# Kernel tuning notes

Measured on AMD Instinct MI355X. Metric: run time of the kernel, lower is better.

The kernel has to match this reference:

```python
import jax, jax.numpy as jnp
import numpy as np

N_NODES = 50000
N_EDGES = 800000
ORIG_FEA = 92
NBR_FEA = 41
HID = 64
N_CONV = 3
BN_EPS = 1e-5


def setup_inputs() -> dict:
    key = jax.random.key(0)
    ks = jax.random.split(key, 16)
    s = 0.05
    inp = {
        "x": jax.random.normal(ks[0], (N_NODES, ORIG_FEA), dtype=jnp.float32),
        "edge_attr": jax.random.normal(ks[1], (N_EDGES, NBR_FEA), dtype=jnp.float32),
        "edge_index": jax.random.randint(ks[2], (2, N_EDGES), 0, N_NODES, dtype=jnp.int64),
        # embedding1 / embedding2
        "W1": jax.random.normal(ks[3], (ORIG_FEA, HID), dtype=jnp.float32) * s,
        "b1": jnp.zeros((HID,), dtype=jnp.float32),
        "W2": jax.random.normal(ks[4], (NBR_FEA, HID), dtype=jnp.float32) * s,
        "b2": jnp.zeros((HID,), dtype=jnp.float32),
        # CGConv lin_f / lin_s per layer, stacked [n_conv, 3*HID, HID]
        "Wf": jax.random.normal(ks[5], (N_CONV, 3 * HID, HID), dtype=jnp.float32) * s,
        "bf": jnp.zeros((N_CONV, HID), dtype=jnp.float32),
        "Ws": jax.random.normal(ks[6], (N_CONV, 3 * HID, HID), dtype=jnp.float32) * s,
        "bs": jnp.zeros((N_CONV, HID), dtype=jnp.float32),
        # BatchNorm1d per layer (training mode: batch statistics)
        "gamma": jnp.ones((N_CONV, HID), dtype=jnp.float32),
        "beta": jnp.zeros((N_CONV, HID), dtype=jnp.float32),
    }
    return inp


def _cgconv(x, e, src, tgt, Wf, bf, Ws, bs):
    # z_ij = [x_i (target), x_j (source), e_ij]  -> [E, 3H]
    z = jnp.concatenate([x[tgt], x[src], e], axis=-1)
    gate = jax.nn.sigmoid(z @ Wf + bf)
    core = jax.nn.softplus(z @ Ws + bs)
    msg = gate * core  # [E, H]
    agg = jax.ops.segment_sum(msg, tgt, num_segments=x.shape[0])
    return x + agg  # residual


def _batchnorm(x, gamma, beta):
    mean = jnp.mean(x, axis=0)
    var = jnp.mean(jnp.square(x - mean), axis=0)  # biased var (torch BN training)
    return (x - mean) * jax.lax.rsqrt(var + BN_EPS) * gamma + beta


def reference(x, edge_attr, edge_index, W1, b1, W2, b2, Wf, bf, Ws, bs, gamma, beta):
    src, tgt = edge_index[0], edge_index[1]
    h = x @ W1 + b1                 # embedding1: [N, H]
    e = edge_attr @ W2 + b2         # embedding2: [E, H]
    for i in range(N_CONV):
        h = _cgconv(h, e, src, tgt, Wf[i], bf[i], Ws[i], bs[i])
        h = _batchnorm(h, gamma[i], beta[i])
        if i < N_CONV - 1:
            h = jax.nn.relu(h)
        # drop_ratio = 0 -> dropout is identity
    return h
```

## Files before the change

kernel.cpp:

```cpp
#include <hip/hip_runtime.h>
#include <cmath>

#define NNODES 50000
#define NEDGES 800000
#define ORIG_FEA 92
#define NBR_FEA 41
#define HID 64
#define BN_EPS 1e-5f
#define ECOLS 48
#define EMB_BLOCKS 1024

typedef __attribute__((ext_vector_type(8))) short short8;
typedef __attribute__((ext_vector_type(4))) float f32x4;
typedef unsigned short ushort;
typedef unsigned int uint;

static __device__ __forceinline__ ushort f2bf(float f) {
    uint u = __float_as_uint(f);
    uint r = u + 0x7fffu + ((u >> 16) & 1u);
    return (ushort)(r >> 16);
}

__global__ void prep(const float* __restrict__ W2, const float* __restrict__ b2,
                     const float* __restrict__ Wf, const float* __restrict__ bf,
                     const float* __restrict__ Ws, const float* __restrict__ bs,
                     ushort* __restrict__ Bpack, ushort* __restrict__ Tpack,
                     float* __restrict__ bcf, float* __restrict__ bcs,
                     float* __restrict__ stats, int* __restrict__ deg) {
    if (blockIdx.x >= 7) {
        int i = (blockIdx.x - 7) * 256 + threadIdx.x;
        if (i < NNODES) deg[i] = 0;
        return;
    }
    if (blockIdx.x == 6) {
        for (int i = threadIdx.x; i < 3 * 128; i += blockDim.x) stats[i] = 0.f;
        return;
    }
    int layer = blockIdx.x >> 1;
    int fs = blockIdx.x & 1;
    const float* Wbig = (fs ? Ws : Wf) + layer * 192 * HID;
    const float* We = Wbig + 128 * HID;
    const float* bvec = (fs ? bs : bf) + layer * HID;
    float* bc = (fs ? bcs : bcf) + layer * HID;
    ushort* Bp = Bpack + layer * 16384 + fs * 8192;
    ushort* Tp = Tpack + layer * 8192 + fs * 4096;

    for (int idx = threadIdx.x; idx < 8192; idx += blockDim.x) {
        int j = idx & 7;
        int lane = (idx >> 3) & 63;
        int ck = (idx >> 9) & 3;
        int tt = (idx >> 11) & 3;
        int k = ck * 32 + ((lane >> 4) * 8) + j;
        int col = tt * 16 + (lane & 15);
        float v = 0.f;
        if (k < 64) v = Wbig[(64 + k) * HID + col];
        else if (k < 64 + NBR_FEA) {
            int r = k - 64;
            float a = 0.f;
            for (int m = 0; m < HID; ++m) a += W2[r * HID + m] * We[m * HID + col];
            v = a;
        }
        Bp[(tt * 4 + ck) * 512 + lane * 8 + j] = f2bf(v);
    }
    for (int idx = threadIdx.x; idx < 4096; idx += blockDim.x) {
        int j = idx & 7;
        int lane = (idx >> 3) & 63;
        int ck = (idx >> 9) & 1;
        int t = (idx >> 10) & 3;
        int k = ck * 32 + ((lane >> 4) * 8) + j;
        int col = t * 16 + (lane & 15);
        Tp[(t * 2 + ck) * 512 + lane * 8 + j] = f2bf(Wbig[k * HID + col]);
    }
    for (int c0 = threadIdx.x; c0 < HID; c0 += blockDim.x) {
        float a = bvec[c0];
        for (int m = 0; m < HID; ++m) a += b2[m] * We[m * HID + c0];
        bc[c0] = a;
    }
}

__global__ void k_hist(const int* __restrict__ eidx, int* __restrict__ deg) {
    int e = blockIdx.x * blockDim.x + threadIdx.x;
    if (e < NEDGES) atomicAdd(&deg[eidx[NEDGES + e]], 1);
}

__global__ void k_blocksum(const int* __restrict__ deg, int* __restrict__ bsum) {
    __shared__ int sh[256];
    int i = blockIdx.x * 256 + threadIdx.x;
    sh[threadIdx.x] = (i < NNODES) ? deg[i] : 0;
    __syncthreads();
    for (int s = 128; s > 0; s >>= 1) {
        if (threadIdx.x < s) sh[threadIdx.x] += sh[threadIdx.x + s];
        __syncthreads();
    }
    if (threadIdx.x == 0) bsum[blockIdx.x] = sh[0];
}

__global__ void k_scanbase(const int* __restrict__ bsum, int* __restrict__ bbase,
                           int* __restrict__ rowptr) {
    __shared__ int sh[256];
    int t = threadIdx.x;
    int v = (t < 196) ? bsum[t] : 0;
    sh[t] = v;
    __syncthreads();
    for (int s = 1; s < 256; s <<= 1) {
        int add = (t >= s) ? sh[t - s] : 0;
        __syncthreads();
        sh[t] += add;
        __syncthreads();
    }
    if (t < 196) bbase[t] = sh[t] - v;
    if (t == 0) rowptr[NNODES] = NEDGES;
}

__global__ void k_writerow(const int* __restrict__ deg, const int* __restrict__ bbase,
                           int* __restrict__ rowptr, int* __restrict__ cursor) {
    __shared__ int sh[256];
    int t = threadIdx.x;
    int i = blockIdx.x * 256 + t;
    int v = (i < NNODES) ? deg[i] : 0;
    sh[t] = v;
    __syncthreads();
    for (int s = 1; s < 256; s <<= 1) {
        int add = (t >= s) ? sh[t - s] : 0;
        __syncthreads();
        sh[t] += add;
        __syncthreads();
    }
    if (i < NNODES) {
        int e = bbase[blockIdx.x] + sh[t] - v;
        rowptr[i] = e;
        cursor[i] = e;
    }
}

__global__ void k_scatterA(const int* __restrict__ eidx, int* __restrict__ cursor,
                           int* __restrict__ posarr, int* __restrict__ srcs) {
    int e = blockIdx.x * blockDim.x + threadIdx.x;
    if (e < NEDGES) {
        int tgt = eidx[NEDGES + e];
        int pos = atomicAdd(&cursor[tgt], 1);
        posarr[e] = pos;
        srcs[pos] = eidx[e];
    }
}

__global__ __launch_bounds__(256) void scatterB_embed(
    const float* __restrict__ ea, const int* __restrict__ posarr,
    ushort* __restrict__ eab_s,
    const float* __restrict__ x, const float* __restrict__ W1,
    const float* __restrict__ b1, float* __restrict__ h,
    ushort* __restrict__ h_bf) {
    if (blockIdx.x < EMB_BLOCKS) {
        int lane = threadIdx.x & 63;
        int wid = (blockIdx.x * blockDim.x + threadIdx.x) >> 6;
        int nw = (EMB_BLOCKS * 256) >> 6;
        float b1v = b1[lane];
        for (int n = wid; n < NNODES; n += nw) {
            const float* xr = x + (long)n * ORIG_FEA;
            float xa = xr[lane];
            float xb = (lane < ORIG_FEA - 64) ? xr[64 + lane] : 0.f;
            float a0 = b1v, a1 = 0.f, a2 = 0.f, a3 = 0.f;
            #pragma unroll
            for (int k = 0; k < 64; k += 4) {
                a0 = fmaf(__shfl(xa, k, 64),     W1[k * HID + lane], a0);
                a1 = fmaf(__shfl(xa, k + 1, 64), W1[(k + 1) * HID + lane], a1);
                a2 = fmaf(__shfl(xa, k + 2, 64), W1[(k + 2) * HID + lane], a2);
                a3 = fmaf(__shfl(xa, k + 3, 64), W1[(k + 3) * HID + lane], a3);
            }
            #pragma unroll
            for (int k = 0; k < ORIG_FEA - 64; k += 4) {
                a0 = fmaf(__shfl(xb, k, 64),     W1[(64 + k) * HID + lane], a0);
                a1 = fmaf(__shfl(xb, k + 1, 64), W1[(65 + k) * HID + lane], a1);
                a2 = fmaf(__shfl(xb, k + 2, 64), W1[(66 + k) * HID + lane], a2);
                a3 = fmaf(__shfl(xb, k + 3, 64), W1[(67 + k) * HID + lane], a3);
            }
            float acc = (a0 + a1) + (a2 + a3);
            h[(long)n * HID + lane] = acc;
            h_bf[(long)n * HID + lane] = f2bf(acc);
        }
        return;
    }
    long idx = (long)(blockIdx.x - EMB_BLOCKS) * blockDim.x + threadIdx.x;
    if (idx >= (long)NEDGES * 6) return;
    int e = (int)(idx / 6);
    int j = (int)(idx - (long)e * 6);
    int p = posarr[e];
    uint w[4];
    #pragma unroll
    for (int m = 0; m < 4; ++m) {
        int k0 = j * 8 + m * 2, k1 = k0 + 1;
        uint u0 = (k0 < NBR_FEA) ? (uint)f2bf(ea[(long)e * NBR_FEA + k0]) : 0u;
        uint u1 = (k1 < NBR_FEA) ? (uint)f2bf(ea[(long)e * NBR_FEA + k1]) : 0u;
        w[m] = u0 | (u1 << 16);
    }
    uint4 o; o.x = w[0]; o.y = w[1]; o.z = w[2]; o.w = w[3];
    *(uint4*)(eab_s + (long)p * ECOLS + j * 8) = o;
}

__global__ __launch_bounds__(256) void proj_mfma(
    const ushort* __restrict__ h_bf, const ushort* __restrict__ Tpack_l,
    const float* __restrict__ bcf_l, const float* __restrict__ bcs_l,
    float* __restrict__ Ttgt) {
    int lane = threadIdx.x & 63;
    int cc = lane & 15;
    int g = lane >> 4;
    short8 Bf[4][2], Bs[4][2];
    #pragma unroll
    for (int t = 0; t < 4; ++t)
        #pragma unroll
        for (int ck = 0; ck < 2; ++ck) {
            Bf[t][ck] = *(const short8*)(Tpack_l + (t * 2 + ck) * 512 + lane * 8);
            Bs[t][ck] = *(const short8*)(Tpack_l + 4096 + (t * 2 + ck) * 512 + lane * 8);
        }
    float bfv[4], bsv[4];
    #pragma unroll
    for (int t = 0; t < 4; ++t) {
        bfv[t] = bcf_l[t * 16 + cc];
        bsv[t] = bcs_l[t * 16 + cc];
    }
    int wid = (blockIdx.x * blockDim.x + threadIdx.x) >> 6;
    int nw = (gridDim.x * blockDim.x) >> 6;
    for (int nb = wid; nb < NNODES / 16; nb += nw) {
        long base = (long)nb * 16;
        long row = base + cc;
        short8 A0 = *(const short8*)(h_bf + row * 64 + g * 8);
        short8 A1 = *(const short8*)(h_bf + row * 64 + 32 + g * 8);
        f32x4 accf[4], accs[4];
        f32x4 z4 = {0.f, 0.f, 0.f, 0.f};
        #pragma unroll
        for (int t = 0; t < 4; ++t) {
            accf[t] = __builtin_amdgcn_mfma_f32_16x16x32_bf16(A0, Bf[t][0], z4, 0, 0, 0);
            accs[t] = __builtin_amdgcn_mfma_f32_16x16x32_bf16(A0, Bs[t][0], z4, 0, 0, 0);
        }
        #pragma unroll
        for (int t = 0; t < 4; ++t) {
            accf[t] = __builtin_amdgcn_mfma_f32_16x16x32_bf16(A1, Bf[t][1], accf[t], 0, 0, 0);
            accs[t] = __builtin_amdgcn_mfma_f32_16x16x32_bf16(A1, Bs[t][1], accs[t], 0, 0, 0);
        }
        #pragma unroll
        for (int r = 0; r < 4; ++r) {
            long node = base + g * 4 + r;
            f32x4 vf = {accf[0][r] + bfv[0], accf[1][r] + bfv[1],
                        accf[2][r] + bfv[2], accf[3][r] + bfv[3]};
            f32x4 vs = {accs[0][r] + bsv[0], accs[1][r] + bsv[1],
                        accs[2][r] + bsv[2], accs[3][r] + bsv[3]};
            *(f32x4*)(Ttgt + node * 128 + cc * 4) = vf;
            *(f32x4*)(Ttgt + node * 128 + 64 + cc * 4) = vs;
        }
    }
}

__global__ __launch_bounds__(256, 2) void edge_kernel(
    const ushort* __restrict__ eab_s, const int* __restrict__ srcs,
    const int* __restrict__ rowptr, const ushort* __restrict__ h_bf,
    const float* __restrict__ h, const float* __restrict__ Ttgt,
    const ushort* __restrict__ Bpack, float* __restrict__ agg,
    float* __restrict__ stats) {
    int lane = threadIdx.x & 63;
    int q = lane >> 4;
    int c = lane & 15;
    int wid = (blockIdx.x * blockDim.x + threadIdx.x) >> 6;
    int nw = (gridDim.x * blockDim.x) >> 6;
    const short8 z8 = {0, 0, 0, 0, 0, 0, 0, 0};

    short8 B[8][4];
    #pragma unroll
    for (int t = 0; t < 8; ++t)
        #pragma unroll
        for (int ck = 0; ck < 4; ++ck)
            B[t][ck] = *(const short8*)(Bpack + ((t * 4 + ck) * 512 + lane * 8));

    float st1 = 0.f, st2 = 0.f;
    int tn = wid;
    int r0 = 0, r1 = 0, svAll = 0;
    short8 A0, A1, A2, A3;
    if (tn < NNODES) {
        r0 = rowptr[tn]; r1 = rowptr[tn + 1];
        int e = r0 + lane; if (e > NEDGES - 1) e = NEDGES - 1;
        svAll = srcs[e];
        int sv = __shfl(svAll, c, 64);
        int ei = r0 + c; if (ei > NEDGES - 1) ei = NEDGES - 1;
        const short8* hrow = (const short8*)(h_bf + (long)sv * 64);
        const ushort* erow = eab_s + (long)ei * ECOLS;
        A0 = hrow[q]; A1 = hrow[4 + q];
        A2 = *(const short8*)(erow + q * 8);
        A3 = z8;
        if (q < 2) A3 = *(const short8*)(erow + 32 + q * 8);
    }

    while (tn < NNODES) {
        int tn2 = tn + nw;
        int r0n = 0, r1n = 0;
        if (tn2 < NNODES) { r0n = rowptr[tn2]; r1n = rowptr[tn2 + 1]; }
        f32x4 tf = *(const f32x4*)(Ttgt + (long)tn * 128 + 4 * c);
        f32x4 ts = *(const f32x4*)(Ttgt + (long)tn * 128 + 64 + 4 * c);
        int d = r1 - r0;
        int nch = (d + 15) >> 4;
        float vs0 = 0.f, vs1 = 0.f, vs2 = 0.f, vs3 = 0.f;

        if (nch == 0) {
            int e = r0n + lane; if (e > NEDGES - 1) e = NEDGES - 1;
            svAll = srcs[e];
            int sv = __shfl(svAll, c, 64);
            int ei = r0n + c; if (ei > NEDGES - 1) ei = NEDGES - 1;
            const short8* hrow = (const short8*)(h_bf + (long)sv * 64);
            const ushort* erow = eab_s + (long)ei * ECOLS;
            A0 = hrow[q]; A1 = hrow[4 + q];
            A2 = *(const short8*)(erow + q * 8);
            A3 = z8;
            if (q < 2) A3 = *(const short8*)(erow + 32 + q * 8);
        } else {
            for (int ci = 0; ci < nch; ++ci) {
                int sv, ei;
                int nidx = ci + 1;
                if (nidx < nch) {
                    if ((nidx & 3) == 0) {
                        int e = r0 + nidx * 16 + lane;
                        if (e > NEDGES - 1) e = NEDGES - 1;
                        svAll = srcs[e];
                    }
                    sv = __shfl(svAll, ((nidx & 3) << 4) + c, 64);
                    ei = r0 + nidx * 16 + c;
                    if (ei > NEDGES - 1) ei = NEDGES - 1;
                } else {
                    int e = r0n + lane; if (e > NEDGES - 1) e = NEDGES - 1;
                    svAll = srcs[e];
                    sv = __shfl(svAll, c, 64);
                    ei = r0n + c; if (ei > NEDGES - 1) ei = NEDGES - 1;
                }
                const short8* hrow = (const short8*)(h_bf + (long)sv * 64);
                const ushort* erow = eab_s + (long)ei * ECOLS;
                short8 N0 = hrow[q], N1 = hrow[4 + q];
                short8 N2 = *(const short8*)(erow + q * 8);
                short8 N3 = z8;
                if (q < 2) N3 = *(const short8*)(erow + 32 + q * 8);

                f32x4 accf[4], accs[4];
                f32x4 z4 = {0.f, 0.f, 0.f, 0.f};
                __builtin_amdgcn_s_setprio(1);
                #pragma unroll
                for (int t = 0; t < 4; ++t) {
                    accf[t] = __builtin_amdgcn_mfma_f32_16x16x32_bf16(A0, B[t][0], z4, 0, 0, 0);
                    accs[t] = __builtin_amdgcn_mfma_f32_16x16x32_bf16(A0, B[t + 4][0], z4, 0, 0, 0);
                }
                #pragma unroll
                for (int t = 0; t < 4; ++t) {
                    accf[t] = __builtin_amdgcn_mfma_f32_16x16x32_bf16(A1, B[t][1], accf[t], 0, 0, 0);
                    accs[t] = __builtin_amdgcn_mfma_f32_16x16x32_bf16(A1, B[t + 4][1], accs[t], 0, 0, 0);
                }
                #pragma unroll
                for (int t = 0; t < 4; ++t) {
                    accf[t] = __builtin_amdgcn_mfma_f32_16x16x32_bf16(A2, B[t][2], accf[t], 0, 0, 0);
                    accs[t] = __builtin_amdgcn_mfma_f32_16x16x32_bf16(A2, B[t + 4][2], accs[t], 0, 0, 0);
                }
                #pragma unroll
                for (int t = 0; t < 4; ++t) {
                    accf[t] = __builtin_amdgcn_mfma_f32_16x16x32_bf16(A3, B[t][3], accf[t], 0, 0, 0);
                    accs[t] = __builtin_amdgcn_mfma_f32_16x16x32_bf16(A3, B[t + 4][3], accs[t], 0, 0, 0);
                }
                __builtin_amdgcn_s_setprio(0);

                int base = ci * 16 + q * 4;
                #pragma unroll
                for (int r = 0; r < 4; ++r) {
                    bool valid = (base + r) < d;
                    #pragma unroll
                    for (int t = 0; t < 4; ++t) {
                        float f = accf[t][r] + tf[t];
                        float s = accs[t][r] + ts[t];
                        float g = __builtin_amdgcn_rcpf(1.f + __expf(-f));
                        float sp = fmaxf(s, 0.f) + __logf(1.f + __expf(-fabsf(s)));
                        float msg = valid ? g * sp : 0.f;
                        if (t == 0) vs0 += msg;
                        else if (t == 1) vs1 += msg;
                        else if (t == 2) vs2 += msg;
                        else vs3 += msg;
                    }
                }
                A0 = N0; A1 = N1; A2 = N2; A3 = N3;
            }
        }
        vs0 += __shfl_xor(vs0, 16, 64); vs0 += __shfl_xor(vs0, 32, 64);
        vs1 += __shfl_xor(vs1, 16, 64); vs1 += __shfl_xor(vs1, 32, 64);
        vs2 += __shfl_xor(vs2, 16, 64); vs2 += __shfl_xor(vs2, 32, 64);
        vs3 += __shfl_xor(vs3, 16, 64); vs3 += __shfl_xor(vs3, 32, 64);
        float out = (q == 0) ? vs0 : (q == 1) ? vs1 : (q == 2) ? vs2 : vs3;
        agg[(long)tn * 64 + lane] = out;
        float v = h[(long)tn * 64 + lane] + out;
        st1 += v;
        st2 = fmaf(v, v, st2);

        tn = tn2; r0 = r0n; r1 = r1n;
    }

    __shared__ float ls[4][64], lq[4][64];
    int w = threadIdx.x >> 6;
    ls[w][lane] = st1; lq[w][lane] = st2;
    __syncthreads();
    if (threadIdx.x < 64) {
        float t1 = ls[0][lane] + ls[1][lane] + ls[2][lane] + ls[3][lane];
        float t2 = lq[0][lane] + lq[1][lane] + lq[2][lane] + lq[3][lane];
        atomicAdd(&stats[lane], t1);
        atomicAdd(&stats[64 + lane], t2);
    }
}

__global__ __launch_bounds__(256) void bnproj(
    float* __restrict__ h, const float* __restrict__ agg,
    const float* __restrict__ stats, const float* __restrict__ gamma,
    const float* __restrict__ beta, ushort* __restrict__ h_bf,
    const ushort* __restrict__ Tpack_l, const float* __restrict__ bcf_l,
    const float* __restrict__ bcs_l, float* __restrict__ Ttgt) {
    int lane = threadIdx.x & 63;
    int cc = lane & 15;
    int g = lane >> 4;
    short8 Bf[4][2], Bs[4][2];
    #pragma unroll
    for (int t = 0; t < 4; ++t)
        #pragma unroll
        for (int ck = 0; ck < 2; ++ck) {
            Bf[t][ck] = *(const short8*)(Tpack_l + (t * 2 + ck) * 512 + lane * 8);
            Bs[t][ck] = *(const short8*)(Tpack_l + 4096 + (t * 2 + ck) * 512 + lane * 8);
        }
    float bfv[4], bsv[4];
    #pragma unroll
    for (int t = 0; t < 4; ++t) {
        bfv[t] = bcf_l[t * 16 + cc];
        bsv[t] = bcs_l[t * 16 + cc];
    }
    const float invn = 1.f / (float)NNODES;
    float sc[16], sh[16];
    #pragma unroll
    for (int m = 0; m < 16; ++m) {
        int ch = (m < 8) ? (g * 8 + m) : (32 + g * 8 + (m - 8));
        float mu = stats[ch] * invn;
        float va = stats[64 + ch] * invn - mu * mu;
        float s = rsqrtf(va + BN_EPS) * gamma[ch];
        sc[m] = s;
        sh[m] = beta[ch] - mu * s;
    }
    int wid = (blockIdx.x * blockDim.x + threadIdx.x) >> 6;
    int nw = (gridDim.x * blockDim.x) >> 6;
    for (int nb = wid; nb < NNODES / 16; nb += nw) {
        long base = (long)nb * 16;
        long row = base + cc;
        float* hr = h + row * 64;
        const float* ar = agg + row * 64;
        float y[16];
        #pragma unroll
        for (int half = 0; half < 2; ++half) {
            int col = half * 32 + g * 8;
            f32x4 hv0 = *(const f32x4*)(hr + col);
            f32x4 hv1 = *(const f32x4*)(hr + col + 4);
            f32x4 av0 = *(const f32x4*)(ar + col);
            f32x4 av1 = *(const f32x4*)(ar + col + 4);
            #pragma unroll
            for (int m = 0; m < 4; ++m) {
                float t0 = (hv0[m] + av0[m]) * sc[half * 8 + m] + sh[half * 8 + m];
                float t1 = (hv1[m] + av1[m]) * sc[half * 8 + 4 + m] + sh[half * 8 + 4 + m];
                y[half * 8 + m] = fmaxf(t0, 0.f);
                y[half * 8 + 4 + m] = fmaxf(t1, 0.f);
            }
        }
        f32x4 w0 = {y[0], y[1], y[2], y[3]},   w1 = {y[4], y[5], y[6], y[7]};
        f32x4 w2 = {y[8], y[9], y[10], y[11]}, w3 = {y[12], y[13], y[14], y[15]};
        *(f32x4*)(hr + g * 8) = w0;       *(f32x4*)(hr + g * 8 + 4) = w1;
        *(f32x4*)(hr + 32 + g * 8) = w2;  *(f32x4*)(hr + 32 + g * 8 + 4) = w3;
        uint u[8];
        #pragma unroll
        for (int m = 0; m < 8; ++m)
            u[m] = (uint)f2bf(y[m * 2]) | ((uint)f2bf(y[m * 2 + 1]) << 16);
        uint4 p0; p0.x = u[0]; p0.y = u[1]; p0.z = u[2]; p0.w = u[3];
        uint4 p1; p1.x = u[4]; p1.y = u[5]; p1.z = u[6]; p1.w = u[7];
        *(uint4*)(h_bf + row * 64 + g * 8) = p0;
        *(uint4*)(h_bf + row * 64 + 32 + g * 8) = p1;
        short8 A0 = *reinterpret_cast<short8*>(&p0);
        short8 A1 = *reinterpret_cast<short8*>(&p1);

        f32x4 accf[4], accs[4];
        f32x4 z4 = {0.f, 0.f, 0.f, 0.f};
        #pragma unroll
        for (int t = 0; t < 4; ++t) {
            accf[t] = __builtin_amdgcn_mfma_f32_16x16x32_bf16(A0, Bf[t][0], z4, 0, 0, 0);
            accs[t] = __builtin_amdgcn_mfma_f32_16x16x32_bf16(A0, Bs[t][0], z4, 0, 0, 0);
        }
        #pragma unroll
        for (int t = 0; t < 4; ++t) {
            accf[t] = __builtin_amdgcn_mfma_f32_16x16x32_bf16(A1, Bf[t][1], accf[t], 0, 0, 0);
            accs[t] = __builtin_amdgcn_mfma_f32_16x16x32_bf16(A1, Bs[t][1], accs[t], 0, 0, 0);
        }
        #pragma unroll
        for (int r = 0; r < 4; ++r) {
            long node = base + g * 4 + r;
            f32x4 vf = {accf[0][r] + bfv[0], accf[1][r] + bfv[1],
                        accf[2][r] + bfv[2], accf[3][r] + bfv[3]};
            f32x4 vs = {accs[0][r] + bsv[0], accs[1][r] + bsv[1],
                        accs[2][r] + bsv[2], accs[3][r] + bsv[3]};
            *(f32x4*)(Ttgt + node * 128 + cc * 4) = vf;
            *(f32x4*)(Ttgt + node * 128 + 64 + cc * 4) = vs;
        }
    }
}

__global__ __launch_bounds__(256) void bn_final(
    float* __restrict__ h, const float* __restrict__ agg,
    const float* __restrict__ stats, const float* __restrict__ gamma,
    const float* __restrict__ beta) {
    int tid = blockIdx.x * blockDim.x + threadIdx.x;
    int nth = gridDim.x * blockDim.x;
    const float invn = 1.f / (float)NNODES;
    int cb = (tid & 15) * 4;
    f32x4 sc, sh;
    #pragma unroll
    for (int j = 0; j < 4; ++j) {
        float m = stats[cb + j] * invn;
        float v = stats[64 + cb + j] * invn - m * m;
        float s = rsqrtf(v + BN_EPS) * gamma[cb + j];
        sc[j] = s;
        sh[j] = beta[cb + j] - m * s;
    }
    for (long i = tid; i < (long)NNODES * 16; i += nth) {
        f32x4 v = ((const f32x4*)h)[i];
        f32x4 a = ((const f32x4*)agg)[i];
        f32x4 y;
        #pragma unroll
        for (int j = 0; j < 4; ++j) y[j] = (v[j] + a[j]) * sc[j] + sh[j];
        ((f32x4*)h)[i] = y;
    }
}

extern "C" void kernel_launch(void* const* d_in, const int* in_sizes, int n_in,
                              void* d_out, int out_size, void* d_ws, size_t ws_size,
                              hipStream_t stream) {
    const float* x    = (const float*)d_in[0];
    const float* ea   = (const float*)d_in[1];
    const int*   eidx = (const int*)d_in[2];
    const float* W1   = (const float*)d_in[3];
    const float* b1   = (const float*)d_in[4];
    const float* W2   = (const float*)d_in[5];
    const float* b2   = (const float*)d_in[6];
    const float* Wf   = (const float*)d_in[7];
    const float* bf   = (const float*)d_in[8];
    const float* Ws   = (const float*)d_in[9];
    const float* bs   = (const float*)d_in[10];
    const float* gamma= (const float*)d_in[11];
    const float* beta = (const float*)d_in[12];
    float* h = (float*)d_out;

    char* wb = (char*)d_ws;
    auto align = [&]() { wb = (char*)(((size_t)wb + 255) & ~(size_t)255); };
    ushort* Bpack = (ushort*)wb;  wb += 3 * 8 * 4 * 512 * sizeof(ushort); align();
    ushort* Tpack = (ushort*)wb;  wb += 3 * 2 * 4 * 2 * 512 * sizeof(ushort); align();
    float* bcf   = (float*)wb;    wb += 3 * HID * sizeof(float);
    float* bcs   = (float*)wb;    wb += 3 * HID * sizeof(float);
    float* stats = (float*)wb;    wb += 3 * 2 * HID * sizeof(float); align();
    int* deg     = (int*)wb;      wb += NNODES * sizeof(int);
    int* rowptr  = (int*)wb;      wb += (NNODES + 1) * sizeof(int);
    int* cursor  = (int*)wb;      wb += NNODES * sizeof(int);
    int* bsum    = (int*)wb;      wb += 256 * sizeof(int);
    int* bbase   = (int*)wb;      wb += 256 * sizeof(int); align();
    int* posarr  = (int*)wb;      wb += NEDGES * sizeof(int);
    int* srcs    = (int*)wb;      wb += NEDGES * sizeof(int);
    align();
    float* Ttgt  = (float*)wb;    wb += (size_t)NNODES * 128 * sizeof(float);
    float* agg   = (float*)wb;    wb += (size_t)NNODES * HID * sizeof(float);
    ushort* h_bf = (ushort*)wb;   wb += (size_t)NNODES * HID * sizeof(ushort);
    ushort* eab_s= (ushort*)wb;   wb += (size_t)NEDGES * ECOLS * sizeof(ushort);

    prep<<<203, 256, 0, stream>>>(W2, b2, Wf, bf, Ws, bs, Bpack, Tpack, bcf, bcs,
                                  stats, deg);
    k_hist<<<(NEDGES + 255) / 256, 256, 0, stream>>>(eidx, deg);
    k_blocksum<<<196, 256, 0, stream>>>(deg, bsum);
    k_scanbase<<<1, 256, 0, stream>>>(bsum, bbase, rowptr);
    k_writerow<<<196, 256, 0, stream>>>(deg, bbase, rowptr, cursor);
    k_scatterA<<<(NEDGES + 255) / 256, 256, 0, stream>>>(eidx, cursor, posarr, srcs);
    scatterB_embed<<<EMB_BLOCKS + (NEDGES * 6 + 255) / 256, 256, 0, stream>>>(
        ea, posarr, eab_s, x, W1, b1, h, h_bf);
    proj_mfma<<<1024, 256, 0, stream>>>(h_bf, Tpack, bcf, bcs, Ttgt);

    for (int i = 0; i < 3; ++i) {
        edge_kernel<<<2048, 256, 0, stream>>>(eab_s, srcs, rowptr, h_bf, h, Ttgt,
                                              Bpack + i * 16384, agg, stats + i * 128);
        if (i < 2)
            bnproj<<<1024, 256, 0, stream>>>(h, agg, stats + i * 128, gamma + i * HID,
                                             beta + i * HID, h_bf,
                                             Tpack + (i + 1) * 8192,
                                             bcf + (i + 1) * HID, bcs + (i + 1) * HID,
                                             Ttgt);
        else
            bn_final<<<2048, 256, 0, stream>>>(h, agg, stats + i * 128,
                                               gamma + i * HID, beta + i * HID);
    }
}
```

Before: 832.0 us.

## Fuse edge-attr bf16 scatter into scatterA and move node embedding into prep

The edge-attribute bf16 conversion and reordering now happens in the same kernel that assigns each edge's CSR slot. This removes the posarr intermediate array and one kernel launch. The node embedding (x@W1) moves into the prep kernel, and the weight-packing work is split across four blocks per layer and gate instead of one. In exchange, each thread now handles a full 41-float edge row, so its loads and stores are strided and less coalesced, and register pressure rises.

```diff
diff --git a/kernel.cpp b/kernel.cpp
--- a/kernel.cpp
+++ b/kernel.cpp
@@ -8,7 +8,6 @@
 #define HID 64
 #define BN_EPS 1e-5f
 #define ECOLS 48
-#define EMB_BLOCKS 1024
 
 typedef __attribute__((ext_vector_type(8))) short short8;
 typedef __attribute__((ext_vector_type(4))) float f32x4;
@@ -21,139 +20,23 @@
     return (ushort)(r >> 16);
 }
 
-__global__ void prep(const float* __restrict__ W2, const float* __restrict__ b2,
-                     const float* __restrict__ Wf, const float* __restrict__ bf,
-                     const float* __restrict__ Ws, const float* __restrict__ bs,
-                     ushort* __restrict__ Bpack, ushort* __restrict__ Tpack,
-                     float* __restrict__ bcf, float* __restrict__ bcs,
-                     float* __restrict__ stats, int* __restrict__ deg) {
-    if (blockIdx.x >= 7) {
-        int i = (blockIdx.x - 7) * 256 + threadIdx.x;
-        if (i < NNODES) deg[i] = 0;
-        return;
-    }
-    if (blockIdx.x == 6) {
-        for (int i = threadIdx.x; i < 3 * 128; i += blockDim.x) stats[i] = 0.f;
-        return;
-    }
-    int layer = blockIdx.x >> 1;
-    int fs = blockIdx.x & 1;
-    const float* Wbig = (fs ? Ws : Wf) + layer * 192 * HID;
-    const float* We = Wbig + 128 * HID;
-    const float* bvec = (fs ? bs : bf) + layer * HID;
-    float* bc = (fs ? bcs : bcf) + layer * HID;
-    ushort* Bp = Bpack + layer * 16384 + fs * 8192;
-    ushort* Tp = Tpack + layer * 8192 + fs * 4096;
-
-    for (int idx = threadIdx.x; idx < 8192; idx += blockDim.x) {
-        int j = idx & 7;
-        int lane = (idx >> 3) & 63;
-        int ck = (idx >> 9) & 3;
-        int tt = (idx >> 11) & 3;
-        int k = ck * 32 + ((lane >> 4) * 8) + j;
-        int col = tt * 16 + (lane & 15);
-        float v = 0.f;
-        if (k < 64) v = Wbig[(64 + k) * HID + col];
-        else if (k < 64 + NBR_FEA) {
-            int r = k - 64;
-            float a = 0.f;
-            for (int m = 0; m < HID; ++m) a += W2[r * HID + m] * We[m * HID + col];
-            v = a;
-        }
-        Bp[(tt * 4 + ck) * 512 + lane * 8 + j] = f2bf(v);
-    }
-    for (int idx = threadIdx.x; idx < 4096; idx += blockDim.x) {
-        int j = idx & 7;
-        int lane = (idx >> 3) & 63;
-        int ck = (idx >> 9) & 1;
-        int t = (idx >> 10) & 3;
-        int k = ck * 32 + ((lane >> 4) * 8) + j;
-        int col = t * 16 + (lane & 15);
-        Tp[(t * 2 + ck) * 512 + lane * 8 + j] = f2bf(Wbig[k * HID + col]);
-    }
-    for (int c0 = threadIdx.x; c0 < HID; c0 += blockDim.x) {
-        float a = bvec[c0];
-        for (int m = 0; m < HID; ++m) a += b2[m] * We[m * HID + c0];
-        bc[c0] = a;
-    }
-}
-
-__global__ void k_hist(const int* __restrict__ eidx, int* __restrict__ deg) {
-    int e = blockIdx.x * blockDim.x + threadIdx.x;
-    if (e < NEDGES) atomicAdd(&deg[eidx[NEDGES + e]], 1);
-}
-
-__global__ void k_blocksum(const int* __restrict__ deg, int* __restrict__ bsum) {
-    __shared__ int sh[256];
-    int i = blockIdx.x * 256 + threadIdx.x;
-    sh[threadIdx.x] = (i < NNODES) ? deg[i] : 0;
-    __syncthreads();
-    for (int s = 128; s > 0; s >>= 1) {
-        if (threadIdx.x < s) sh[threadIdx.x] += sh[threadIdx.x + s];
-        __syncthreads();
-    }
-    if (threadIdx.x == 0) bsum[blockIdx.x] = sh[0];
-}
-
-__global__ void k_scanbase(const int* __restrict__ bsum, int* __restrict__ bbase,
-                           int* __restrict__ rowptr) {
-    __shared__ int sh[256];
-    int t = threadIdx.x;
-    int v = (t < 196) ? bsum[t] : 0;
-    sh[t] = v;
-    __syncthreads();
-    for (int s = 1; s < 256; s <<= 1) {
-        int add = (t >= s) ? sh[t - s] : 0;
-        __syncthreads();
-        sh[t] += add;
-        __syncthreads();
-    }
-    if (t < 196) bbase[t] = sh[t] - v;
-    if (t == 0) rowptr[NNODES] = NEDGES;
-}
-
-__global__ void k_writerow(const int* __restrict__ deg, const int* __restrict__ bbase,
-                           int* __restrict__ rowptr, int* __restrict__ cursor) {
-    __shared__ int sh[256];
-    int t = threadIdx.x;
-    int i = blockIdx.x * 256 + t;
-    int v = (i < NNODES) ? deg[i] : 0;
-    sh[t] = v;
-    __syncthreads();
-    for (int s = 1; s < 256; s <<= 1) {
-        int add = (t >= s) ? sh[t - s] : 0;
-        __syncthreads();
-        sh[t] += add;
-        __syncthreads();
-    }
-    if (i < NNODES) {
-        int e = bbase[blockIdx.x] + sh[t] - v;
-        rowptr[i] = e;
-        cursor[i] = e;
-    }
-}
-
-__global__ void k_scatterA(const int* __restrict__ eidx, int* __restrict__ cursor,
-                           int* __restrict__ posarr, int* __restrict__ srcs) {
-    int e = blockIdx.x * blockDim.x + threadIdx.x;
-    if (e < NEDGES) {
-        int tgt = eidx[NEDGES + e];
-        int pos = atomicAdd(&cursor[tgt], 1);
-        posarr[e] = pos;
-        srcs[pos] = eidx[e];
-    }
-}
-
-__global__ __launch_bounds__(256) void scatterB_embed(
-    const float* __restrict__ ea, const int* __restrict__ posarr,
-    ushort* __restrict__ eab_s,
+#define EMBED_BASE 221
+#define EMBED_BLOCKS 1024
+
+__global__ __launch_bounds__(256) void prep_embed(
+    const float* __restrict__ W2, const float* __restrict__ b2,
+    const float* __restrict__ Wf, const float* __restrict__ bf,
+    const float* __restrict__ Ws, const float* __restrict__ bs,
+    ushort* __restrict__ Bpack, ushort* __restrict__ Tpack,
+    float* __restrict__ bcf, float* __restrict__ bcs,
+    float* __restrict__ stats, int* __restrict__ deg,
     const float* __restrict__ x, const float* __restrict__ W1,
     const float* __restrict__ b1, float* __restrict__ h,
     ushort* __restrict__ h_bf) {
-    if (blockIdx.x < EMB_BLOCKS) {
+    if (blockIdx.x >= EMBED_BASE) {
         int lane = threadIdx.x & 63;
-        int wid = (blockIdx.x * blockDim.x + threadIdx.x) >> 6;
-        int nw = (EMB_BLOCKS * 256) >> 6;
+        int wid = (((int)blockIdx.x - EMBED_BASE) * 256 + (int)threadIdx.x) >> 6;
+        int nw = (EMBED_BLOCKS * 256) >> 6;
         float b1v = b1[lane];
         for (int n = wid; n < NNODES; n += nw) {
             const float* xr = x + (long)n * ORIG_FEA;
@@ -180,21 +63,144 @@
         }
         return;
     }
-    long idx = (long)(blockIdx.x - EMB_BLOCKS) * blockDim.x + threadIdx.x;
-    if (idx >= (long)NEDGES * 6) return;
-    int e = (int)(idx / 6);
-    int j = (int)(idx - (long)e * 6);
-    int p = posarr[e];
-    uint w[4];
-    #pragma unroll
-    for (int m = 0; m < 4; ++m) {
-        int k0 = j * 8 + m * 2, k1 = k0 + 1;
-        uint u0 = (k0 < NBR_FEA) ? (uint)f2bf(ea[(long)e * NBR_FEA + k0]) : 0u;
-        uint u1 = (k1 < NBR_FEA) ? (uint)f2bf(ea[(long)e * NBR_FEA + k1]) : 0u;
-        w[m] = u0 | (u1 << 16);
-    }
-    uint4 o; o.x = w[0]; o.y = w[1]; o.z = w[2]; o.w = w[3];
-    *(uint4*)(eab_s + (long)p * ECOLS + j * 8) = o;
+    if (blockIdx.x >= 25) {
+        int i = ((int)blockIdx.x - 25) * 256 + (int)threadIdx.x;
+        if (i < NNODES) deg[i] = 0;
+        return;
+    }
+    if (blockIdx.x == 24) {
+        for (int i = threadIdx.x; i < 3 * 128; i += blockDim.x) stats[i] = 0.f;
+        return;
+    }
+    int group = blockIdx.x >> 2;
+    int quarter = blockIdx.x & 3;
+    int layer = group >> 1;
+    int fs = group & 1;
+    const float* Wbig = (fs ? Ws : Wf) + layer * 192 * HID;
+    const float* We = Wbig + 128 * HID;
+    const float* bvec = (fs ? bs : bf) + layer * HID;
+    float* bc = (fs ? bcs : bcf) + layer * HID;
+    ushort* Bp = Bpack + layer * 16384 + fs * 8192;
+    ushort* Tp = Tpack + layer * 8192 + fs * 4096;
+
+    for (int idx = quarter * 2048 + threadIdx.x; idx < (quarter + 1) * 2048;
+         idx += blockDim.x) {
+        int j = idx & 7;
+        int lane = (idx >> 3) & 63;
+        int ck = (idx >> 9) & 3;
+        int tt = (idx >> 11) & 3;
+        int k = ck * 32 + ((lane >> 4) * 8) + j;
+        int col = tt * 16 + (lane & 15);
+        float v = 0.f;
+        if (k < 64) v = Wbig[(64 + k) * HID + col];
+        else if (k < 64 + NBR_FEA) {
+            int r = k - 64;
+            float a = 0.f;
+            for (int m = 0; m < HID; ++m) a += W2[r * HID + m] * We[m * HID + col];
+            v = a;
+        }
+        Bp[(tt * 4 + ck) * 512 + lane * 8 + j] = f2bf(v);
+    }
+    for (int idx = quarter * 1024 + threadIdx.x; idx < (quarter + 1) * 1024;
+         idx += blockDim.x) {
+        int j = idx & 7;
+        int lane = (idx >> 3) & 63;
+        int ck = (idx >> 9) & 1;
+        int t = (idx >> 10) & 3;
+        int k = ck * 32 + ((lane >> 4) * 8) + j;
+        int col = t * 16 + (lane & 15);
+        Tp[(t * 2 + ck) * 512 + lane * 8 + j] = f2bf(Wbig[k * HID + col]);
+    }
+    if (quarter == 3) {
+        for (int c0 = threadIdx.x; c0 < HID; c0 += blockDim.x) {
+            float a = bvec[c0];
+            for (int m = 0; m < HID; ++m) a += b2[m] * We[m * HID + c0];
+            bc[c0] = a;
+        }
+    }
+}
+
+__global__ void k_hist(const int* __restrict__ eidx, int* __restrict__ deg) {
+    int e = blockIdx.x * blockDim.x + threadIdx.x;
+    if (e < NEDGES) atomicAdd(&deg[eidx[NEDGES + e]], 1);
+}
+
+__global__ void k_blocksum(const int* __restrict__ deg, int* __restrict__ bsum) {
+    __shared__ int sh[256];
+    int i = blockIdx.x * 256 + threadIdx.x;
+    sh[threadIdx.x] = (i < NNODES) ? deg[i] : 0;
+    __syncthreads();
+    for (int s = 128; s > 0; s >>= 1) {
+        if (threadIdx.x < s) sh[threadIdx.x] += sh[threadIdx.x + s];
+        __syncthreads();
+    }
+    if (threadIdx.x == 0) bsum[blockIdx.x] = sh[0];
+}
+
+__global__ void k_scanbase(const int* __restrict__ bsum, int* __restrict__ bbase,
+                           int* __restrict__ rowptr) {
+    __shared__ int sh[256];
+    int t = threadIdx.x;
+    int v = (t < 196) ? bsum[t] : 0;
+    sh[t] = v;
+    __syncthreads();
+    for (int s = 1; s < 256; s <<= 1) {
+        int add = (t >= s) ? sh[t - s] : 0;
+        __syncthreads();
+        sh[t] += add;
+        __syncthreads();
+    }
+    if (t < 196) bbase[t] = sh[t] - v;
+    if (t == 0) rowptr[NNODES] = NEDGES;
+}
+
+__global__ void k_writerow(const int* __restrict__ deg, const int* __restrict__ bbase,
+                           int* __restrict__ rowptr, int* __restrict__ cursor) {
+    __shared__ int sh[256];
+    int t = threadIdx.x;
+    int i = blockIdx.x * 256 + t;
+    int v = (i < NNODES) ? deg[i] : 0;
+    sh[t] = v;
+    __syncthreads();
+    for (int s = 1; s < 256; s <<= 1) {
+        int add = (t >= s) ? sh[t - s] : 0;
+        __syncthreads();
+        sh[t] += add;
+        __syncthreads();
+    }
+    if (i < NNODES) {
+        int e = bbase[blockIdx.x] + sh[t] - v;
+        rowptr[i] = e;
+        cursor[i] = e;
+    }
+}
+
+__global__ __launch_bounds__(256) void scatterA_eab(
+    const int* __restrict__ eidx, int* __restrict__ cursor,
+    int* __restrict__ srcs, const float* __restrict__ ea,
+    ushort* __restrict__ eab_s) {
+    int e = blockIdx.x * blockDim.x + threadIdx.x;
+    if (e >= NEDGES) return;
+    const float* row = ea + (long)e * NBR_FEA;
+    float a[NBR_FEA];
+    #pragma unroll
+    for (int k = 0; k < NBR_FEA; ++k) a[k] = row[k];
+    int tgt = eidx[NEDGES + e];
+    int pos = atomicAdd(&cursor[tgt], 1);
+    srcs[pos] = eidx[e];
+    uint u[24];
+    #pragma unroll
+    for (int m = 0; m < 20; ++m)
+        u[m] = (uint)f2bf(a[2 * m]) | ((uint)f2bf(a[2 * m + 1]) << 16);
+    u[20] = (uint)f2bf(a[40]);
+    u[21] = 0u; u[22] = 0u; u[23] = 0u;
+    uint4* dst = (uint4*)(eab_s + (long)pos * ECOLS);
+    #pragma unroll
+    for (int m = 0; m < 6; ++m) {
+        uint4 o; o.x = u[4 * m]; o.y = u[4 * m + 1];
+        o.z = u[4 * m + 2]; o.w = u[4 * m + 3];
+        dst[m] = o;
+    }
 }
 
 __global__ __launch_bounds__(256) void proj_mfma(
@@ -559,7 +565,6 @@
     int* cursor  = (int*)wb;      wb += NNODES * sizeof(int);
     int* bsum    = (int*)wb;      wb += 256 * sizeof(int);
     int* bbase   = (int*)wb;      wb += 256 * sizeof(int); align();
-    int* posarr  = (int*)wb;      wb += NEDGES * sizeof(int);
     int* srcs    = (int*)wb;      wb += NEDGES * sizeof(int);
     align();
     float* Ttgt  = (float*)wb;    wb += (size_t)NNODES * 128 * sizeof(float);
@@ -567,15 +572,15 @@
     ushort* h_bf = (ushort*)wb;   wb += (size_t)NNODES * HID * sizeof(ushort);
     ushort* eab_s= (ushort*)wb;   wb += (size_t)NEDGES * ECOLS * sizeof(ushort);
 
-    prep<<<203, 256, 0, stream>>>(W2, b2, Wf, bf, Ws, bs, Bpack, Tpack, bcf, bcs,
-                                  stats, deg);
+    prep_embed<<<EMBED_BASE + EMBED_BLOCKS, 256, 0, stream>>>(
+        W2, b2, Wf, bf, Ws, bs, Bpack, Tpack, bcf, bcs, stats, deg,
+        x, W1, b1, h, h_bf);
     k_hist<<<(NEDGES + 255) / 256, 256, 0, stream>>>(eidx, deg);
     k_blocksum<<<196, 256, 0, stream>>>(deg, bsum);
     k_scanbase<<<1, 256, 0, stream>>>(bsum, bbase, rowptr);
     k_writerow<<<196, 256, 0, stream>>>(deg, bbase, rowptr, cursor);
-    k_scatterA<<<(NEDGES + 255) / 256, 256, 0, stream>>>(eidx, cursor, posarr, srcs);
-    scatterB_embed<<<EMB_BLOCKS + (NEDGES * 6 + 255) / 256, 256, 0, stream>>>(
-        ea, posarr, eab_s, x, W1, b1, h, h_bf);
+    scatterA_eab<<<(NEDGES + 255) / 256, 256, 0, stream>>>(eidx, cursor, srcs,
+                                                           ea, eab_s);
     proj_mfma<<<1024, 256, 0, stream>>>(h_bf, Tpack, bcf, bcs, Ttgt);
 
     for (int i = 0; i < 3; ++i) {
```

Measured after the change: 765.4 us. 1.09x faster.
